# Optimization experiments

Hardware: AMD Instinct MI355X
Metric: run time of the kernel (lower is better)

The kernel has to match this reference:

```python
import jax, jax.numpy as jnp
import numpy as np

N = 4096
IN_F = 512
OUT_F = 512


def setup_inputs() -> dict:
    key = jax.random.key(0)
    k1, k2, k3, k4 = jax.random.split(key, 4)
    x = jax.random.normal(k1, (N, IN_F), dtype=jnp.float32)
    adj = jax.random.uniform(k2, (N, N), dtype=jnp.float32)
    # linear params (torch nn.Linear default init: U(-1/sqrt(fan_in), 1/sqrt(fan_in)))
    bound = 1.0 / np.sqrt(IN_F)
    W = jax.random.uniform(k3, (OUT_F, IN_F), minval=-bound, maxval=bound, dtype=jnp.float32)
    b = jax.random.uniform(k4, (OUT_F,), minval=-bound, maxval=bound, dtype=jnp.float32)
    return {"x": x, "adj": adj, "W": W, "b": b}


def reference(x, adj, W, b):
    # adj_hat = adj + I
    adj_hat = adj + jnp.eye(adj.shape[0], dtype=adj.dtype)
    # deg is diagonal with 1/sqrt(rowsum); deg @ adj @ deg == d[:,None] * adj * d[None,:]
    d = 1.0 / jnp.sqrt(adj_hat.sum(axis=1))  # [N]
    norm_adj = d[:, None] * adj_hat * d[None, :]  # [N, N]
    h = norm_adj @ x  # [N, in_features]
    return h @ W.T + b  # [N, out_features]
```

## Files before the change

### kernel.cpp

```cpp
#include <hip/hip_runtime.h>
#include <cstdint>

#define NN 4096
#define FF 512

typedef short bf16x8 __attribute__((ext_vector_type(8)));
typedef float f32x4 __attribute__((ext_vector_type(4)));

__device__ __forceinline__ uint16_t f2bf(float f) {
    uint32_t u = __builtin_bit_cast(uint32_t, f);
    u += 0x7FFFu + ((u >> 16) & 1u);
    return (uint16_t)(u >> 16);
}

__global__ __launch_bounds__(256) void k_prep(const float* __restrict__ adj,
                                              float* __restrict__ d,
                                              uint16_t* __restrict__ Abf) {
    const int row  = blockIdx.x * 4 + (threadIdx.x >> 6);
    const int lane = threadIdx.x & 63;
    const float4* p = (const float4*)(adj + (size_t)row * NN);
    float4 v[16];
    float s = 0.f;
#pragma unroll
    for (int i = 0; i < 16; ++i) {
        v[i] = p[lane + i * 64];
        s += (v[i].x + v[i].y) + (v[i].z + v[i].w);
    }
#pragma unroll
    for (int off = 1; off < 64; off <<= 1) s += __shfl_xor(s, off);
    const float di = rsqrtf(s + 1.0f);
    if (lane == 0) d[row] = di;
    uint16_t* outp = Abf + (size_t)row * NN;
#pragma unroll
    for (int i = 0; i < 16; ++i) {
        const int cb = (lane + i * 64) * 4;
        float a0 = v[i].x * di, a1 = v[i].y * di, a2 = v[i].z * di, a3 = v[i].w * di;
        if (cb + 0 == row) a0 += di;
        if (cb + 1 == row) a1 += di;
        if (cb + 2 == row) a2 += di;
        if (cb + 3 == row) a3 += di;
        ushort4 o;
        o.x = f2bf(a0); o.y = f2bf(a1); o.z = f2bf(a2); o.w = f2bf(a3);
        *(ushort4*)(outp + cb) = o;
    }
}

__global__ __launch_bounds__(256) void k_xt(const float* __restrict__ x,
                                            const float* __restrict__ d,
                                            uint16_t* __restrict__ yT) {
    __shared__ uint16_t t[64][72];
    const int k0 = blockIdx.x * 64;
    const int n0 = blockIdx.y * 64;
    const int tid = threadIdx.x;
    const int r   = tid >> 4;
    const int c4  = tid & 15;
#pragma unroll
    for (int pass = 0; pass < 4; ++pass) {
        const int row = pass * 16 + r;
        float4 v = *(const float4*)(x + (size_t)(k0 + row) * FF + n0 + c4 * 4);
        const float dk = d[k0 + row];
        t[c4 * 4 + 0][row] = f2bf(v.x * dk);
        t[c4 * 4 + 1][row] = f2bf(v.y * dk);
        t[c4 * 4 + 2][row] = f2bf(v.z * dk);
        t[c4 * 4 + 3][row] = f2bf(v.w * dk);
    }
    __syncthreads();
#pragma unroll
    for (int pass = 0; pass < 2; ++pass) {
        const int cid = pass * 256 + tid;
        const int n  = cid >> 3;
        const int ch = cid & 7;
        *(uint4*)(yT + (size_t)(n0 + n) * NN + k0 + ch * 8) = *(const uint4*)&t[n][ch * 8];
    }
}

__global__ __launch_bounds__(256) void k_wc(const float* __restrict__ W,
                                            uint16_t* __restrict__ Wbf) {
    const size_t t4 = (size_t)blockIdx.x * 256 + threadIdx.x;
    float4 v = *(const float4*)(W + t4 * 4);
    ushort4 o;
    o.x = f2bf(v.x); o.y = f2bf(v.y); o.z = f2bf(v.z); o.w = f2bf(v.w);
    *(ushort4*)(Wbf + t4 * 4) = o;
}

template <int K, bool OUT_BF16>
__global__ __launch_bounds__(256, 2) void k_gemm(const uint16_t* __restrict__ A,
                                                 const uint16_t* __restrict__ Bt,
                                                 const float* __restrict__ bias,
                                                 uint16_t* __restrict__ outb,
                                                 float* __restrict__ outf) {
    constexpr int NT = K / 64;
    __shared__ uint16_t As[4][64 * 64];
    __shared__ uint16_t Bs[4][64 * 64];

    const int id   = blockIdx.x;
    const int xcd  = id & 7;
    const int slot = id >> 3;
    const int n_t  = slot & 7;
    const int m_t  = xcd * 8 + (slot >> 3);
    const int m0 = m_t * 64;
    const int n0 = n_t * 64;

    const int tid  = threadIdx.x;
    const int w    = tid >> 6;
    const int lane = tid & 63;
    const int wm = w >> 1, wn = w & 1;

    f32x4 acc[2][2] = {};

    auto STAGE = [&](int t, int buf) {
#pragma unroll
        for (int i = 0; i < 2; ++i) {
            const int boff = w * 2048 + i * 1024 + lane * 16;
            const int row  = boff >> 7;
            const int q    = (boff >> 4) & 7;
            const int c    = q ^ (row & 7);
            const uint16_t* srcA = A  + (size_t)(m0 + row) * K + t * 64 + c * 8;
            const uint16_t* srcB = Bt + (size_t)(n0 + row) * K + t * 64 + c * 8;
            __builtin_amdgcn_global_load_lds(
                (const __attribute__((address_space(1))) void*)srcA,
                (__attribute__((address_space(3))) void*)&As[buf][(w * 2048 + i * 1024) >> 1],
                16, 0, 0);
            __builtin_amdgcn_global_load_lds(
                (const __attribute__((address_space(1))) void*)srcB,
                (__attribute__((address_space(3))) void*)&Bs[buf][(w * 2048 + i * 1024) >> 1],
                16, 0, 0);
        }
    };

    auto COMPUTE = [&](int buf) {
#pragma unroll
        for (int kk = 0; kk < 2; ++kk) {
            bf16x8 af[2], bfr[2];
#pragma unroll
            for (int mf = 0; mf < 2; ++mf) {
                const int m  = wm * 32 + mf * 16 + (lane & 15);
                const int ch = (kk * 4 + (lane >> 4)) ^ (m & 7);
                af[mf] = *(const bf16x8*)&As[buf][m * 64 + ch * 8];
            }
#pragma unroll
            for (int nf = 0; nf < 2; ++nf) {
                const int n  = wn * 32 + nf * 16 + (lane & 15);
                const int ch = (kk * 4 + (lane >> 4)) ^ (n & 7);
                bfr[nf] = *(const bf16x8*)&Bs[buf][n * 64 + ch * 8];
            }
#pragma unroll
            for (int mf = 0; mf < 2; ++mf)
#pragma unroll
                for (int nf = 0; nf < 2; ++nf)
                    acc[mf][nf] = __builtin_amdgcn_mfma_f32_16x16x32_bf16(
                        af[mf], bfr[nf], acc[mf][nf], 0, 0, 0);
        }
    };

    STAGE(0, 0);
    STAGE(1, 1);
    STAGE(2, 2);

    for (int t = 0; t < NT - 3; ++t) {
        STAGE(t + 3, (t + 3) & 3);
        asm volatile("s_waitcnt vmcnt(12)" ::: "memory");
        __builtin_amdgcn_s_barrier();
        COMPUTE(t & 3);
        __builtin_amdgcn_s_barrier();
    }
    asm volatile("s_waitcnt vmcnt(8)" ::: "memory");
    __builtin_amdgcn_s_barrier();
    COMPUTE((NT - 3) & 3);
    asm volatile("s_waitcnt vmcnt(4)" ::: "memory");
    __builtin_amdgcn_s_barrier();
    COMPUTE((NT - 2) & 3);
    asm volatile("s_waitcnt vmcnt(0)" ::: "memory");
    __builtin_amdgcn_s_barrier();
    COMPUTE((NT - 1) & 3);

#pragma unroll
    for (int mf = 0; mf < 2; ++mf) {
#pragma unroll
        for (int nf = 0; nf < 2; ++nf) {
            const int rbase = m0 + wm * 32 + mf * 16 + ((lane >> 4) << 2);
            const int col   = n0 + wn * 32 + nf * 16 + (lane & 15);
#pragma unroll
            for (int r = 0; r < 4; ++r) {
                const size_t idx = (size_t)(rbase + r) * FF + col;
                if constexpr (OUT_BF16) {
                    outb[idx] = f2bf(acc[mf][nf][r]);
                } else {
                    outf[idx] = acc[mf][nf][r] + bias[col];
                }
            }
        }
    }
}

extern "C" void kernel_launch(void* const* d_in, const int* in_sizes, int n_in,
                              void* d_out, int out_size, void* d_ws, size_t ws_size,
                              hipStream_t stream) {
    const float* x   = (const float*)d_in[0];
    const float* adj = (const float*)d_in[1];
    const float* W   = (const float*)d_in[2];
    const float* b   = (const float*)d_in[3];
    float* out = (float*)d_out;

    char* ws = (char*)d_ws;
    float*    d_   = (float*)ws;
    uint16_t* Abf  = (uint16_t*)(ws + 65536);
    uint16_t* yT   = Abf + (size_t)NN * NN;
    uint16_t* hbf  = yT  + (size_t)FF * NN;
    uint16_t* Wbf  = hbf + (size_t)NN * FF;

    k_prep<<<NN / 4, 256, 0, stream>>>(adj, d_, Abf);
    k_xt<<<dim3(NN / 64, FF / 64), 256, 0, stream>>>(x, d_, yT);
    k_wc<<<FF * FF / 4 / 256, 256, 0, stream>>>(W, Wbf);
    k_gemm<NN, true><<<(NN / 64) * (FF / 64), 256, 0, stream>>>(Abf, yT, nullptr, hbf, nullptr);
    k_gemm<FF, false><<<(NN / 64) * (FF / 64), 256, 0, stream>>>(hbf, Wbf, b, nullptr, out);
}
```

Baseline: 69.98 us.

## Reassociate GCN as adj·(xWᵀ) with split-K atomic GEMMs and 32x32 MFMA tiles

Reorders the computation to first form z = x·Wᵀ, then multiply the normalized adjacency by the row-scaled transpose of z. Row scaling by d is applied in the epilogue instead of in the adjacency conversion. Both GEMMs now use a templated kernel with larger tiles, 512 threads, 32x32x16 MFMAs and split-K accumulation through float atomics into zeroed outputs. The intent is better tile reuse and more parallelism for the large-K GEMM. It adds memsets, atomic traffic, an extra fp32 intermediate and a nondeterministic summation order.

```diff
diff --git a/kernel.cpp b/kernel.cpp
--- a/kernel.cpp
+++ b/kernel.cpp
@@ -5,7 +5,7 @@
 #define FF 512
 
 typedef short bf16x8 __attribute__((ext_vector_type(8)));
-typedef float f32x4 __attribute__((ext_vector_type(4)));
+typedef float f32x16 __attribute__((ext_vector_type(16)));
 
 __device__ __forceinline__ uint16_t f2bf(float f) {
     uint32_t u = __builtin_bit_cast(uint32_t, f);
@@ -34,44 +34,24 @@
 #pragma unroll
     for (int i = 0; i < 16; ++i) {
         const int cb = (lane + i * 64) * 4;
-        float a0 = v[i].x * di, a1 = v[i].y * di, a2 = v[i].z * di, a3 = v[i].w * di;
-        if (cb + 0 == row) a0 += di;
-        if (cb + 1 == row) a1 += di;
-        if (cb + 2 == row) a2 += di;
-        if (cb + 3 == row) a3 += di;
+        float a0 = v[i].x, a1 = v[i].y, a2 = v[i].z, a3 = v[i].w;
+        if (cb + 0 == row) a0 += 1.0f;
+        if (cb + 1 == row) a1 += 1.0f;
+        if (cb + 2 == row) a2 += 1.0f;
+        if (cb + 3 == row) a3 += 1.0f;
         ushort4 o;
         o.x = f2bf(a0); o.y = f2bf(a1); o.z = f2bf(a2); o.w = f2bf(a3);
         *(ushort4*)(outp + cb) = o;
     }
 }
 
-__global__ __launch_bounds__(256) void k_xt(const float* __restrict__ x,
-                                            const float* __restrict__ d,
-                                            uint16_t* __restrict__ yT) {
-    __shared__ uint16_t t[64][72];
-    const int k0 = blockIdx.x * 64;
-    const int n0 = blockIdx.y * 64;
-    const int tid = threadIdx.x;
-    const int r   = tid >> 4;
-    const int c4  = tid & 15;
-#pragma unroll
-    for (int pass = 0; pass < 4; ++pass) {
-        const int row = pass * 16 + r;
-        float4 v = *(const float4*)(x + (size_t)(k0 + row) * FF + n0 + c4 * 4);
-        const float dk = d[k0 + row];
-        t[c4 * 4 + 0][row] = f2bf(v.x * dk);
-        t[c4 * 4 + 1][row] = f2bf(v.y * dk);
-        t[c4 * 4 + 2][row] = f2bf(v.z * dk);
-        t[c4 * 4 + 3][row] = f2bf(v.w * dk);
-    }
-    __syncthreads();
-#pragma unroll
-    for (int pass = 0; pass < 2; ++pass) {
-        const int cid = pass * 256 + tid;
-        const int n  = cid >> 3;
-        const int ch = cid & 7;
-        *(uint4*)(yT + (size_t)(n0 + n) * NN + k0 + ch * 8) = *(const uint4*)&t[n][ch * 8];
-    }
+__global__ __launch_bounds__(256) void k_xc(const float* __restrict__ x,
+                                            uint16_t* __restrict__ xbf) {
+    const size_t t4 = (size_t)blockIdx.x * 256 + threadIdx.x;
+    float4 v = *(const float4*)(x + t4 * 4);
+    ushort4 o;
+    o.x = f2bf(v.x); o.y = f2bf(v.y); o.z = f2bf(v.z); o.w = f2bf(v.w);
+    *(ushort4*)(xbf + t4 * 4) = o;
 }
 
 __global__ __launch_bounds__(256) void k_wc(const float* __restrict__ W,
@@ -83,72 +63,122 @@
     *(ushort4*)(Wbf + t4 * 4) = o;
 }
 
-template <int K, bool OUT_BF16>
-__global__ __launch_bounds__(256, 2) void k_gemm(const uint16_t* __restrict__ A,
-                                                 const uint16_t* __restrict__ Bt,
-                                                 const float* __restrict__ bias,
-                                                 uint16_t* __restrict__ outb,
-                                                 float* __restrict__ outf) {
-    constexpr int NT = K / 64;
-    __shared__ uint16_t As[4][64 * 64];
-    __shared__ uint16_t Bs[4][64 * 64];
+__global__ __launch_bounds__(256) void k_zt(const float* __restrict__ z32,
+                                            const float* __restrict__ d,
+                                            uint16_t* __restrict__ zdT) {
+    __shared__ uint16_t t[64][72];
+    const int k0 = blockIdx.x * 64;
+    const int n0 = blockIdx.y * 64;
+    const int tid = threadIdx.x;
+    const int r   = tid >> 4;
+    const int c4  = tid & 15;
+#pragma unroll
+    for (int pass = 0; pass < 4; ++pass) {
+        const int row = pass * 16 + r;
+        float4 v = *(const float4*)(z32 + (size_t)(k0 + row) * FF + n0 + c4 * 4);
+        const float dk = d[k0 + row];
+        t[c4 * 4 + 0][row] = f2bf(v.x * dk);
+        t[c4 * 4 + 1][row] = f2bf(v.y * dk);
+        t[c4 * 4 + 2][row] = f2bf(v.z * dk);
+        t[c4 * 4 + 3][row] = f2bf(v.w * dk);
+    }
+    __syncthreads();
+#pragma unroll
+    for (int pass = 0; pass < 2; ++pass) {
+        const int cid = pass * 256 + tid;
+        const int n  = cid >> 3;
+        const int ch = cid & 7;
+        *(uint4*)(zdT + (size_t)(n0 + n) * NN + k0 + ch * 8) = *(const uint4*)&t[n][ch * 8];
+    }
+}
+
+template <int BM, int BN, int K, int SPLITK, int MODE>
+__global__ __launch_bounds__(512, 2) void k_mm(const uint16_t* __restrict__ A,
+                                               const uint16_t* __restrict__ Bt,
+                                               const float* __restrict__ bias,
+                                               const float* __restrict__ dvec,
+                                               float* __restrict__ outf) {
+    constexpr int MT    = NN / BM;
+    constexpr int NTC   = FF / BN;
+    constexpr int KSLEN = K / SPLITK;
+    constexpr int NT    = KSLEN / 32;
+    constexpr int MTX   = MT / 8;
+    constexpr int MF    = BM / 64;
+    constexpr int NF    = BN / 128;
+    constexpr int LPT_A = BM / 128;
+    constexpr int LPT_B = BN / 128;
+    constexpr int LPT   = LPT_A + LPT_B;
+
+    __shared__ uint16_t As[4][BM * 32];
+    __shared__ uint16_t Bs[4][BN * 32];
 
     const int id   = blockIdx.x;
-    const int xcd  = id & 7;
     const int slot = id >> 3;
-    const int n_t  = slot & 7;
-    const int m_t  = xcd * 8 + (slot >> 3);
-    const int m0 = m_t * 64;
-    const int n0 = n_t * 64;
+    const int mt   = (id & 7) * MTX + slot / (NTC * SPLITK);
+    const int rem  = slot % (NTC * SPLITK);
+    const int nt   = rem % NTC;
+    const int ks   = rem / NTC;
+    const int m0 = mt * BM;
+    const int n0 = nt * BN;
+    const int k0 = ks * KSLEN;
 
     const int tid  = threadIdx.x;
     const int w    = tid >> 6;
     const int lane = tid & 63;
-    const int wm = w >> 1, wn = w & 1;
-
-    f32x4 acc[2][2] = {};
+    const int wm = w >> 2, wn = w & 3;
+
+    f32x16 acc[MF][NF] = {};
 
     auto STAGE = [&](int t, int buf) {
-#pragma unroll
-        for (int i = 0; i < 2; ++i) {
-            const int boff = w * 2048 + i * 1024 + lane * 16;
-            const int row  = boff >> 7;
-            const int q    = (boff >> 4) & 7;
-            const int c    = q ^ (row & 7);
-            const uint16_t* srcA = A  + (size_t)(m0 + row) * K + t * 64 + c * 8;
-            const uint16_t* srcB = Bt + (size_t)(n0 + row) * K + t * 64 + c * 8;
+        const int ktb = k0 + t * 32;
+#pragma unroll
+        for (int i = 0; i < LPT_A; ++i) {
+            const int boff = i * 8192 + tid * 16;
+            const int row  = boff >> 6;
+            const int q    = (boff >> 4) & 3;
+            const int c    = (q + 4 - ((row >> 1) & 3)) & 3;
+            const uint16_t* src = A + (size_t)(m0 + row) * K + ktb + c * 8;
             __builtin_amdgcn_global_load_lds(
-                (const __attribute__((address_space(1))) void*)srcA,
-                (__attribute__((address_space(3))) void*)&As[buf][(w * 2048 + i * 1024) >> 1],
+                (const __attribute__((address_space(1))) void*)src,
+                (__attribute__((address_space(3))) void*)&As[buf][boff >> 1],
                 16, 0, 0);
+        }
+#pragma unroll
+        for (int i = 0; i < LPT_B; ++i) {
+            const int boff = i * 8192 + tid * 16;
+            const int row  = boff >> 6;
+            const int q    = (boff >> 4) & 3;
+            const int c    = (q + 4 - ((row >> 1) & 3)) & 3;
+            const uint16_t* src = Bt + (size_t)(n0 + row) * K + ktb + c * 8;
             __builtin_amdgcn_global_load_lds(
-                (const __attribute__((address_space(1))) void*)srcB,
-                (__attribute__((address_space(3))) void*)&Bs[buf][(w * 2048 + i * 1024) >> 1],
+                (const __attribute__((address_space(1))) void*)src,
+                (__attribute__((address_space(3))) void*)&Bs[buf][boff >> 1],
                 16, 0, 0);
         }
     };
 
     auto COMPUTE = [&](int buf) {
 #pragma unroll
-        for (int kk = 0; kk < 2; ++kk) {
-            bf16x8 af[2], bfr[2];
-#pragma unroll
-            for (int mf = 0; mf < 2; ++mf) {
-                const int m  = wm * 32 + mf * 16 + (lane & 15);
-                const int ch = (kk * 4 + (lane >> 4)) ^ (m & 7);
-                af[mf] = *(const bf16x8*)&As[buf][m * 64 + ch * 8];
+        for (int ksl = 0; ksl < 2; ++ksl) {
+            const int cl = ksl * 2 + (lane >> 5);
+            bf16x8 af[MF], bfr[NF];
+#pragma unroll
+            for (int mf = 0; mf < MF; ++mf) {
+                const int r = wm * (BM / 2) + mf * 32 + (lane & 31);
+                const int s = (cl + ((r >> 1) & 3)) & 3;
+                af[mf] = *(const bf16x8*)&As[buf][r * 32 + s * 8];
             }
 #pragma unroll
-            for (int nf = 0; nf < 2; ++nf) {
-                const int n  = wn * 32 + nf * 16 + (lane & 15);
-                const int ch = (kk * 4 + (lane >> 4)) ^ (n & 7);
-                bfr[nf] = *(const bf16x8*)&Bs[buf][n * 64 + ch * 8];
+            for (int nf = 0; nf < NF; ++nf) {
+                const int r = wn * (BN / 4) + nf * 32 + (lane & 31);
+                const int s = (cl + ((r >> 1) & 3)) & 3;
+                bfr[nf] = *(const bf16x8*)&Bs[buf][r * 32 + s * 8];
             }
 #pragma unroll
-            for (int mf = 0; mf < 2; ++mf)
-#pragma unroll
-                for (int nf = 0; nf < 2; ++nf)
-                    acc[mf][nf] = __builtin_amdgcn_mfma_f32_16x16x32_bf16(
+            for (int mf = 0; mf < MF; ++mf)
+#pragma unroll
+                for (int nf = 0; nf < NF; ++nf)
+                    acc[mf][nf] = __builtin_amdgcn_mfma_f32_32x32x16_bf16(
                         af[mf], bfr[nf], acc[mf][nf], 0, 0, 0);
         }
     };
@@ -159,35 +189,39 @@
 
     for (int t = 0; t < NT - 3; ++t) {
         STAGE(t + 3, (t + 3) & 3);
-        asm volatile("s_waitcnt vmcnt(12)" ::: "memory");
+        if constexpr (LPT == 4) asm volatile("s_waitcnt vmcnt(12)" ::: "memory");
+        else                    asm volatile("s_waitcnt vmcnt(6)" ::: "memory");
         __builtin_amdgcn_s_barrier();
         COMPUTE(t & 3);
         __builtin_amdgcn_s_barrier();
     }
-    asm volatile("s_waitcnt vmcnt(8)" ::: "memory");
+    if constexpr (LPT == 4) asm volatile("s_waitcnt vmcnt(8)" ::: "memory");
+    else                    asm volatile("s_waitcnt vmcnt(4)" ::: "memory");
     __builtin_amdgcn_s_barrier();
     COMPUTE((NT - 3) & 3);
-    asm volatile("s_waitcnt vmcnt(4)" ::: "memory");
+    if constexpr (LPT == 4) asm volatile("s_waitcnt vmcnt(4)" ::: "memory");
+    else                    asm volatile("s_waitcnt vmcnt(2)" ::: "memory");
     __builtin_amdgcn_s_barrier();
     COMPUTE((NT - 2) & 3);
     asm volatile("s_waitcnt vmcnt(0)" ::: "memory");
     __builtin_amdgcn_s_barrier();
     COMPUTE((NT - 1) & 3);
 
-#pragma unroll
-    for (int mf = 0; mf < 2; ++mf) {
-#pragma unroll
-        for (int nf = 0; nf < 2; ++nf) {
-            const int rbase = m0 + wm * 32 + mf * 16 + ((lane >> 4) << 2);
-            const int col   = n0 + wn * 32 + nf * 16 + (lane & 15);
-#pragma unroll
-            for (int r = 0; r < 4; ++r) {
-                const size_t idx = (size_t)(rbase + r) * FF + col;
-                if constexpr (OUT_BF16) {
-                    outb[idx] = f2bf(acc[mf][nf][r]);
-                } else {
-                    outf[idx] = acc[mf][nf][r] + bias[col];
-                }
+    const int rb = m0 + wm * (BM / 2) + ((lane >> 5) << 2);
+    const int cb = n0 + wn * (BN / 4) + (lane & 31);
+#pragma unroll
+    for (int mf = 0; mf < MF; ++mf) {
+#pragma unroll
+        for (int nf = 0; nf < NF; ++nf) {
+            const int gcol = cb + nf * 32;
+            float bv = 0.f;
+            if constexpr (MODE == 2) { if (ks == 0) bv = bias[gcol]; }
+#pragma unroll
+            for (int r = 0; r < 16; ++r) {
+                const int grow = rb + mf * 32 + (r & 3) + ((r >> 2) << 3);
+                float v = acc[mf][nf][r];
+                if constexpr (MODE == 2) v = v * dvec[grow] + bv;
+                unsafeAtomicAdd(&outf[(size_t)grow * FF + gcol], v);
             }
         }
     }
@@ -205,13 +239,17 @@
     char* ws = (char*)d_ws;
     float*    d_   = (float*)ws;
     uint16_t* Abf  = (uint16_t*)(ws + 65536);
-    uint16_t* yT   = Abf + (size_t)NN * NN;
-    uint16_t* hbf  = yT  + (size_t)FF * NN;
-    uint16_t* Wbf  = hbf + (size_t)NN * FF;
-
+    uint16_t* zdT  = Abf + (size_t)NN * NN;
+    uint16_t* xbf  = zdT + (size_t)FF * NN;
+    uint16_t* Wbf  = xbf + (size_t)NN * FF;
+    float*    z32  = (float*)(Wbf + (size_t)FF * FF);
+
+    hipMemsetAsync(z32, 0, (size_t)NN * FF * sizeof(float), stream);
+    hipMemsetAsync(out, 0, (size_t)NN * FF * sizeof(float), stream);
+    k_wc<<<FF * FF / 1024, 256, 0, stream>>>(W, Wbf);
+    k_xc<<<NN * FF / 1024, 256, 0, stream>>>(x, xbf);
     k_prep<<<NN / 4, 256, 0, stream>>>(adj, d_, Abf);
-    k_xt<<<dim3(NN / 64, FF / 64), 256, 0, stream>>>(x, d_, yT);
-    k_wc<<<FF * FF / 4 / 256, 256, 0, stream>>>(W, Wbf);
-    k_gemm<NN, true><<<(NN / 64) * (FF / 64), 256, 0, stream>>>(Abf, yT, nullptr, hbf, nullptr);
-    k_gemm<FF, false><<<(NN / 64) * (FF / 64), 256, 0, stream>>>(hbf, Wbf, b, nullptr, out);
-}
+    k_mm<128, 128, FF, 2, 0><<<256, 512, 0, stream>>>(xbf, Wbf, nullptr, nullptr, z32);
+    k_zt<<<dim3(NN / 64, FF / 64), 256, 0, stream>>>(z32, d_, zdT);
+    k_mm<256, 256, NN, 8, 2><<<256, 512, 0, stream>>>(Abf, zdT, b, d_, out);
+}
```

After: 121.9 us. 1.74x slower.
